# Kernel optimization log

Hardware: AMD Instinct MI355X
Metric: run time of the kernel (lower is better)

Reference implementation:

```python
import jax, jax.numpy as jnp
import numpy as np

DECAY = 0.1
EPS = 1e-5


def setup_inputs() -> dict:
    key = jax.random.key(0)
    k1, k2, k3, k4 = jax.random.split(key, 4)
    N, K, D = 262144, 1024, 64
    x = jax.random.normal(k1, (N, D), dtype=jnp.float32)
    embed = jax.random.normal(k2, (K, D), dtype=jnp.float32) * 0.01
    cluster_size = jax.random.uniform(k3, (K,), dtype=jnp.float32)
    embed_avg = jax.random.normal(k4, (K, D), dtype=jnp.float32) * 0.01
    return {"x": x, "embed": embed, "cluster_size": cluster_size, "embed_avg": embed_avg}


def reference(x, embed, cluster_size, embed_avg):
    # x: [N, D] flattened latents; embed: [K, D] codebook
    N, D = x.shape
    K = embed.shape[0]

    # Squared Euclidean distance (same argmin as torch.cdist p=2).
    x2 = jnp.sum(x * x, axis=-1, keepdims=True)            # [N, 1]
    e2 = jnp.sum(embed * embed, axis=-1)                   # [K]
    dist = x2 - 2.0 * jnp.einsum('nd,kd->nk', x, embed) + e2[None, :]  # [N, K]
    embed_ind = jnp.argmin(dist, axis=-1)                  # [N] int

    # Quantize: gather nearest codes.
    quantize = embed[embed_ind]                            # [N, D]

    # --- EMA codebook update (no-grad in the original) ---
    xs = jax.lax.stop_gradient(x)
    bins = jax.ops.segment_sum(jnp.ones((N,), dtype=x.dtype), embed_ind,
                               num_segments=K)             # [K] bincount
    embed_sum = jax.ops.segment_sum(xs, embed_ind, num_segments=K)  # [K, D] scatter-add

    cluster_size_new = cluster_size * DECAY + bins * (1.0 - DECAY)
    embed_avg_new = embed_avg * DECAY + embed_sum * (1.0 - DECAY)

    # Laplace smoothing then normalize to get the updated codebook.
    n = jnp.sum(cluster_size_new)
    cs_smoothed = (cluster_size_new + EPS) / (n + K * EPS) * n
    embed_normalized = embed_avg_new / cs_smoothed[:, None]  # [K, D]

    return quantize, embed_ind, cluster_size_new, embed_avg_new, embed_normalized
```

## Files before the change

### kernel.cpp

```cpp
#include <hip/hip_runtime.h>
#include <hip/hip_bf16.h>


#define NROWS 262144
#define KCODES 1024
#define DDIM 64
#define CAPL 8

typedef __attribute__((ext_vector_type(8)))  short short8;
typedef __attribute__((ext_vector_type(16))) float f32x16;

__device__ __forceinline__ unsigned short f2bf(float f) {
    unsigned u = __float_as_uint(f);
    unsigned r = u + 0x7fffu + ((u >> 16) & 1u);
    return (unsigned short)(r >> 16);
}

__global__ __launch_bounds__(256) void vq_prep(
    const float* __restrict__ embed, unsigned short* __restrict__ eb,
    float* __restrict__ e2f, float* __restrict__ enmax2)
{
    const int k = blockIdx.x * 256 + threadIdx.x;
    const float* er = embed + (size_t)k * DDIM;
    float s = 0.f;
    #pragma unroll
    for (int d = 0; d < DDIM; ++d) { float v = er[d]; s = fmaf(v, v, s); }
    e2f[k] = s;
    #pragma unroll
    for (int d = 0; d < DDIM; ++d) eb[(size_t)k * DDIM + d] = f2bf(er[d]);
    atomicMax((int*)enmax2, __float_as_int(s));
}

#define STAGE(H)                                                              \
    _Pragma("unroll")                                                         \
    for (int it = 0; it < 8; ++it) {                                          \
        const int f16  = t + it * 512;                                        \
        const int ch   = f16 >> 8;                                            \
        const int r    = f16 & 255;                                           \
        const int code = r >> 3, slot = r & 7;                                \
        const short8 v = *reinterpret_cast<const short8*>(                    \
            eb + (size_t)(H) * 32768 + (size_t)f16 * 8);                      \
        *reinterpret_cast<short8*>((char*)ebs + ch * 4096 + code * 128 +      \
                                   ((slot ^ (code & 7)) << 4)) = v;           \
    }

#define SWEEP1(E2ARR)                                                         \
    _Pragma("unroll")                                                         \
    for (int ch = 0; ch < 16; ++ch) {                                         \
        short8 bfr[4];                                                        \
        _Pragma("unroll")                                                     \
        for (int i = 0; i < 4; ++i) {                                         \
            const int slot = 2 * i + hi;                                      \
            bfr[i] = *reinterpret_cast<const short8*>(                        \
                (char*)ebs + ch * 4096 + lo * 128 + ((slot ^ (lo & 7)) << 4));\
        }                                                                     \
        const float e2l = E2ARR[ch];                                          \
        f32x16 acc;                                                           \
        _Pragma("unroll")                                                     \
        for (int r = 0; r < 16; ++r) acc[r] = 0.f;                            \
        _Pragma("unroll")                                                     \
        for (int i = 0; i < 4; ++i)                                           \
            acc = __builtin_amdgcn_mfma_f32_32x32x16_bf16(af[i], bfr[i], acc, 0, 0, 0); \
        _Pragma("unroll")                                                     \
        for (int r = 0; r < 16; ++r)                                          \
            best[r] = fminf(best[r], fmaf(-2.f, acc[r], e2l));                \
    }

#define SWEEP2(E2ARR, CBASE)                                                  \
    _Pragma("unroll")                                                         \
    for (int ch = 0; ch < 16; ++ch) {                                         \
        short8 bfr[4];                                                        \
        _Pragma("unroll")                                                     \
        for (int i = 0; i < 4; ++i) {                                         \
            const int slot = 2 * i + hi;                                      \
            bfr[i] = *reinterpret_cast<const short8*>(                        \
                (char*)ebs + ch * 4096 + lo * 128 + ((slot ^ (lo & 7)) << 4));\
        }                                                                     \
        const float e2l = E2ARR[ch];                                          \
        f32x16 acc;                                                           \
        _Pragma("unroll")                                                     \
        for (int r = 0; r < 16; ++r) acc[r] = 0.f;                            \
        _Pragma("unroll")                                                     \
        for (int i = 0; i < 4; ++i)                                           \
            acc = __builtin_amdgcn_mfma_f32_32x32x16_bf16(af[i], bfr[i], acc, 0, 0, 0); \
        _Pragma("unroll")                                                     \
        for (int r = 0; r < 16; ++r) {                                        \
            const float d0 = fmaf(-2.f, acc[r], e2l);                         \
            if (d0 <= best[r]) {                                              \
                const int rr = (r & 3) + 8 * (r >> 2) + 4 * hi;               \
                const int rl = wid * 32 + rr;                                 \
                const int idx = atomicAdd(&cntL[rl], 1);                      \
                if (idx < CAPL) candL[rl][idx] = (CBASE) + ch * 32 + lo;      \
            }                                                                 \
        }                                                                     \
    }

__global__ __launch_bounds__(512, 4) void vq_phaseA(
    const float* __restrict__ x, const unsigned short* __restrict__ eb,
    const float* __restrict__ e2f, const float* __restrict__ enmax2,
    float* __restrict__ out_ind, int* __restrict__ candg, int* __restrict__ cntg,
    int* __restrict__ wl, int* __restrict__ gcount,
    int* __restrict__ wl2, int* __restrict__ gcount2, int* __restrict__ bins_i)
{
    __shared__ __align__(16) unsigned short ebs[32768];
    __shared__ float norm2L[256];
    __shared__ int   cntL[256];
    __shared__ int   candL[256][CAPL];
    __shared__ int   mcount, mbase, mcount2, mbase2;

    const int t    = threadIdx.x;
    const int lane = t & 63;
    const int wid  = t >> 6;
    const int lo   = lane & 31;
    const int hi   = lane >> 5;
    const int rowb = blockIdx.x * 256;
    const int myrow = rowb + wid * 32 + lo;

    short8 af[4];
    float xsq = 0.f;
    {
        const float* xr = x + (size_t)myrow * DDIM;
        #pragma unroll
        for (int i = 0; i < 4; ++i) {
            const float4 a = *reinterpret_cast<const float4*>(xr + 16 * i + 8 * hi);
            const float4 b = *reinterpret_cast<const float4*>(xr + 16 * i + 8 * hi + 4);
            short8 f;
            f[0] = (short)f2bf(a.x); f[1] = (short)f2bf(a.y);
            f[2] = (short)f2bf(a.z); f[3] = (short)f2bf(a.w);
            f[4] = (short)f2bf(b.x); f[5] = (short)f2bf(b.y);
            f[6] = (short)f2bf(b.z); f[7] = (short)f2bf(b.w);
            af[i] = f;
            xsq = fmaf(a.x, a.x, xsq); xsq = fmaf(a.y, a.y, xsq);
            xsq = fmaf(a.z, a.z, xsq); xsq = fmaf(a.w, a.w, xsq);
            xsq = fmaf(b.x, b.x, xsq); xsq = fmaf(b.y, b.y, xsq);
            xsq = fmaf(b.z, b.z, xsq); xsq = fmaf(b.w, b.w, xsq);
        }
    }
    const float n2full = xsq + __shfl_xor(xsq, 32);
    if (hi == 0) norm2L[wid * 32 + lo] = n2full;

    float e2h0[16], e2h1[16];
    #pragma unroll
    for (int c = 0; c < 16; ++c) e2h0[c] = e2f[c * 32 + lo];
    #pragma unroll
    for (int c = 0; c < 16; ++c) e2h1[c] = e2f[(16 + c) * 32 + lo];

    if (t < 256) cntL[t] = 0;
    if (t == 0) { mcount = 0; mcount2 = 0; }
    const float en2 = *enmax2;

    f32x16 best;
    #pragma unroll
    for (int r = 0; r < 16; ++r) best[r] = 3.4e38f;

    STAGE(0)
    __syncthreads();
    SWEEP1(e2h0)
    __syncthreads();
    STAGE(1)
    __syncthreads();
    SWEEP1(e2h1)

    #pragma unroll
    for (int r = 0; r < 16; ++r) {
        float v = best[r];
        v = fminf(v, __shfl_xor(v, 1));  v = fminf(v, __shfl_xor(v, 2));
        v = fminf(v, __shfl_xor(v, 4));  v = fminf(v, __shfl_xor(v, 8));
        v = fminf(v, __shfl_xor(v, 16));
        const int rr = (r & 3) + 8 * (r >> 2) + 4 * hi;
        const float nr2 = norm2L[wid * 32 + rr];
        best[r] = v + 0.015625f * sqrtf(nr2 * en2) + 1e-4f;
    }

    SWEEP2(e2h1, 512)
    __syncthreads();
    STAGE(0)
    __syncthreads();
    SWEEP2(e2h0, 0)
    __syncthreads();

    int my = -1, my2 = -1, c = 0;
    if (t < 256) {
        c = cntL[t];
        if (c == 1) {
            const int code = candL[t][0];
            out_ind[rowb + t] = (float)code;
            atomicAdd(bins_i + code, 1);
        }
        else if (c <= CAPL)   my  = atomicAdd(&mcount, 1);
        else                  my2 = atomicAdd(&mcount2, 1);
    }
    __syncthreads();
    if (t == 0) { mbase = atomicAdd(gcount, mcount); mbase2 = atomicAdd(gcount2, mcount2); }
    __syncthreads();
    if (my >= 0) {
        const int row = rowb + t;
        wl[mbase + my] = row;
        cntg[row] = c;
        #pragma unroll
        for (int j = 0; j < CAPL; ++j)
            if (j < c) candg[row * 8 + j] = candL[t][j];
    }
    if (my2 >= 0) wl2[mbase2 + my2] = rowb + t;
}

__global__ __launch_bounds__(256) void vq_rerank1(
    const float* __restrict__ x, const float* __restrict__ embed,
    const float* __restrict__ e2f, const int* __restrict__ wl,
    const int* __restrict__ gcount, const int* __restrict__ cntg,
    const int* __restrict__ candg, float* __restrict__ out_ind,
    int* __restrict__ bins_i)
{
    const int n = *gcount;
    for (int i = blockIdx.x * 256 + threadIdx.x; i < n; i += gridDim.x * 256) {
        const int row = wl[i];
        float xv[DDIM];
        {
            const float4* xp = reinterpret_cast<const float4*>(x + (size_t)row * DDIM);
            float4 xq[16];
            #pragma unroll
            for (int q = 0; q < 16; ++q) xq[q] = xp[q];
            #pragma unroll
            for (int q = 0; q < 16; ++q) {
                xv[q*4+0] = xq[q].x; xv[q*4+1] = xq[q].y;
                xv[q*4+2] = xq[q].z; xv[q*4+3] = xq[q].w;
            }
        }
        float x2 = 0.f;
        #pragma unroll
        for (int d = 0; d < DDIM; ++d) x2 = fmaf(xv[d], xv[d], x2);

        const int c = cntg[row];
        float bv = 3.4e38f; int bk = 0x7fffffff;
        for (int ci = 0; ci < c; ++ci) {
            const int k = candg[row * 8 + ci];
            const float4* ep = reinterpret_cast<const float4*>(embed + (size_t)k * DDIM);
            float dot = 0.f;
            #pragma unroll
            for (int q = 0; q < 16; ++q) {
                const float4 e4 = ep[q];
                dot = fmaf(xv[q*4+0], e4.x, dot);
                dot = fmaf(xv[q*4+1], e4.y, dot);
                dot = fmaf(xv[q*4+2], e4.z, dot);
                dot = fmaf(xv[q*4+3], e4.w, dot);
            }
            const float dist = (x2 - 2.0f * dot) + e2f[k];
            if (dist < bv || (dist == bv && k < bk)) { bv = dist; bk = k; }
        }
        out_ind[row] = (float)bk;
        atomicAdd(bins_i + bk, 1);
    }
}

__global__ __launch_bounds__(256) void vq_rerank2(
    const float* __restrict__ x, const float* __restrict__ embed,
    const float* __restrict__ e2f, const int* __restrict__ wl2,
    const int* __restrict__ gcount2, float* __restrict__ out_ind,
    int* __restrict__ bins_i)
{
    const int t    = threadIdx.x;
    const int lane = t & 63;
    const int gw   = (blockIdx.x * 256 + t) >> 6;
    const int nw   = (gridDim.x * 256) >> 6;
    const int n    = *gcount2;

    for (int e = gw; e < n; e += nw) {
        const int row = wl2[e];
        float xv[DDIM];
        {
            const float4* xp = reinterpret_cast<const float4*>(x + (size_t)row * DDIM);
            #pragma unroll
            for (int q = 0; q < 16; ++q) {
                const float4 v = xp[q];
                xv[q*4+0] = v.x; xv[q*4+1] = v.y; xv[q*4+2] = v.z; xv[q*4+3] = v.w;
            }
        }
        float x2 = 0.f;
        #pragma unroll
        for (int d = 0; d < DDIM; ++d) x2 = fmaf(xv[d], xv[d], x2);

        float bv = 3.4e38f; int bk = 0x7fffffff;
        for (int k = lane; k < KCODES; k += 64) {
            const float* er = embed + (size_t)k * DDIM;
            float dot = 0.f;
            #pragma unroll
            for (int d = 0; d < DDIM; ++d) dot = fmaf(xv[d], er[d], dot);
            const float dist = (x2 - 2.0f * dot) + e2f[k];
            if (dist < bv) { bv = dist; bk = k; }
        }
        #pragma unroll
        for (int s = 1; s < 64; s <<= 1) {
            const float ov = __shfl_xor(bv, s);
            const int   ok = __shfl_xor(bk, s);
            if (ov < bv || (ov == bv && ok < bk)) { bv = ov; bk = ok; }
        }
        if (lane == 0) { out_ind[row] = (float)bk; atomicAdd(bins_i + bk, 1); }
    }
}

__global__ __launch_bounds__(1024) void vq_prefix(
    const int* __restrict__ bins_i, int* __restrict__ offs, int* __restrict__ cursor)
{
    __shared__ int s[KCODES];
    const int t = threadIdx.x;
    const int b = bins_i[t];
    s[t] = b;
    __syncthreads();
    for (int d = 1; d < KCODES; d <<= 1) {
        const int v = (t >= d) ? s[t - d] : 0;
        __syncthreads();
        s[t] += v;
        __syncthreads();
    }
    const int excl = s[t] - b;
    offs[t] = excl;
    cursor[t] = excl;
}

__global__ __launch_bounds__(256) void vq_scatter(
    const float* __restrict__ out_ind, int* __restrict__ cursor, int* __restrict__ sorted)
{
    const int row  = blockIdx.x * 256 + threadIdx.x;
    const int code = (int)out_ind[row];
    const int pos  = atomicAdd(cursor + code, 1);
    sorted[pos] = (code << 20) | row;
}

__global__ __launch_bounds__(256) void vq_reduce(
    const float* __restrict__ x, const int* __restrict__ sorted,
    float* __restrict__ esum)
{
    const int t = threadIdx.x, lane = t & 63, w = t >> 6;
    const int p0 = (blockIdx.x * 4 + w) * 64;

    int cur = sorted[p0] >> 20;
    float acc = 0.f;
    #pragma unroll 4
    for (int i = 0; i < 64; i += 4) {
        const int4 e4 = *reinterpret_cast<const int4*>(sorted + p0 + i);
        const float v0 = x[(size_t)(e4.x & 0xFFFFF) * DDIM + lane];
        const float v1 = x[(size_t)(e4.y & 0xFFFFF) * DDIM + lane];
        const float v2 = x[(size_t)(e4.z & 0xFFFFF) * DDIM + lane];
        const float v3 = x[(size_t)(e4.w & 0xFFFFF) * DDIM + lane];
        const int c0 = e4.x >> 20, c1 = e4.y >> 20, c2 = e4.z >> 20, c3 = e4.w >> 20;
        if (c0 != cur) { unsafeAtomicAdd(esum + cur * DDIM + lane, acc); acc = 0.f; cur = c0; }
        acc += v0;
        if (c1 != cur) { unsafeAtomicAdd(esum + cur * DDIM + lane, acc); acc = 0.f; cur = c1; }
        acc += v1;
        if (c2 != cur) { unsafeAtomicAdd(esum + cur * DDIM + lane, acc); acc = 0.f; cur = c2; }
        acc += v2;
        if (c3 != cur) { unsafeAtomicAdd(esum + cur * DDIM + lane, acc); acc = 0.f; cur = c3; }
        acc += v3;
    }
    unsafeAtomicAdd(esum + cur * DDIM + lane, acc);
}

__global__ __launch_bounds__(1024) void vq_finalize(
    const float* __restrict__ cluster_size, const float* __restrict__ embed_avg,
    const int* __restrict__ bins_i, float* __restrict__ out_cs,
    float* __restrict__ out_eavg, float* __restrict__ out_enorm)
{
    __shared__ float red[KCODES];
    __shared__ float css[KCODES];
    const int t = threadIdx.x;

    const float csn = cluster_size[t] * 0.1f + (float)bins_i[t] * 0.9f;
    red[t] = csn;
    __syncthreads();
    for (int s = 512; s > 0; s >>= 1) {
        if (t < s) red[t] += red[t + s];
        __syncthreads();
    }
    const float n = red[0];
    out_cs[t] = csn;
    css[t] = (csn + 1e-5f) / (n + (float)(KCODES * 1e-5)) * n;
    __syncthreads();

    #pragma unroll
    for (int i = 0; i < 16; ++i) {
        const int f4 = t + i * 1024;
        const int k  = f4 >> 4;
        const float4 ea = reinterpret_cast<const float4*>(embed_avg)[f4];
        const float4 su = reinterpret_cast<const float4*>(out_eavg)[f4];
        const float  cc = css[k];
        float4 ean, en;
        ean.x = ea.x * 0.1f + su.x * 0.9f; en.x = ean.x / cc;
        ean.y = ea.y * 0.1f + su.y * 0.9f; en.y = ean.y / cc;
        ean.z = ea.z * 0.1f + su.z * 0.9f; en.z = ean.z / cc;
        ean.w = ea.w * 0.1f + su.w * 0.9f; en.w = ean.w / cc;
        reinterpret_cast<float4*>(out_eavg)[f4]  = ean;
        reinterpret_cast<float4*>(out_enorm)[f4] = en;
    }
}

__global__ __launch_bounds__(256) void vq_quant(
    const float* __restrict__ out_ind, const float* __restrict__ embed,
    float* __restrict__ out_q)
{
    __shared__ int inds[256];
    const int t = threadIdx.x;
    const int row0 = blockIdx.x * 256;
    inds[t] = (int)out_ind[row0 + t];
    __syncthreads();
    #pragma unroll
    for (int i = 0; i < 16; ++i) {
        const int f = t + i * 256;
        const int r = f >> 4, dq = f & 15;
        const int code = inds[r];
        const float4 ev = *reinterpret_cast<const float4*>(
            embed + (size_t)code * DDIM + dq * 4);
        *reinterpret_cast<float4*>(out_q + (size_t)(row0 + r) * DDIM + dq * 4) = ev;
    }
}

extern "C" void kernel_launch(void* const* d_in, const int* in_sizes, int n_in,
                              void* d_out, int out_size, void* d_ws, size_t ws_size,
                              hipStream_t stream)
{
    const float* x            = (const float*)d_in[0];
    const float* embed        = (const float*)d_in[1];
    const float* cluster_size = (const float*)d_in[2];
    const float* embed_avg    = (const float*)d_in[3];

    float* out      = (float*)d_out;
    float* out_q    = out;
    float* out_ind  = out_q + (size_t)NROWS * DDIM;
    float* out_cs   = out_ind + NROWS;
    float* out_eavg = out_cs + KCODES;
    float* out_en   = out_eavg + (size_t)KCODES * DDIM;

    unsigned short* eb = (unsigned short*)out_en;
    float* e2f = out_en + 32768;

    int* S      = (int*)out_q;
    int* candg  = S;
    int* cntg   = S + 2097152;
    int* wl     = S + 2359296;
    int* wl2    = S + 2621440;
    int* sorted = S + 2883584;
    int* bins_i = S + 3145728;
    int* gcount = bins_i + KCODES;
    int* gcount2= gcount + 1;
    float* enmax2 = (float*)(gcount2 + 1);
    int* offs   = gcount2 + 2;
    int* cursor = offs + KCODES;

    hipMemsetAsync(bins_i, 0, (KCODES + 3) * sizeof(int), stream);
    hipMemsetAsync(out_eavg, 0, (size_t)KCODES * DDIM * sizeof(float), stream);

    vq_prep    <<<KCODES / 256, 256, 0, stream>>>(embed, eb, e2f, enmax2);
    vq_phaseA  <<<NROWS / 256, 512, 0, stream>>>(x, eb, e2f, enmax2, out_ind,
                                                 candg, cntg, wl, gcount,
                                                 wl2, gcount2, bins_i);
    vq_rerank1 <<<512, 256, 0, stream>>>(x, embed, e2f, wl, gcount, cntg, candg,
                                         out_ind, bins_i);
    vq_rerank2 <<<128, 256, 0, stream>>>(x, embed, e2f, wl2, gcount2, out_ind, bins_i);
    vq_prefix  <<<1, 1024, 0, stream>>>(bins_i, offs, cursor);
    vq_scatter <<<NROWS / 256, 256, 0, stream>>>(out_ind, cursor, sorted);
    vq_reduce  <<<NROWS / 256, 256, 0, stream>>>(x, sorted, out_eavg);
    vq_finalize<<<1, 1024, 0, stream>>>(cluster_size, embed_avg, bins_i,
                                        out_cs, out_eavg, out_en);
    vq_quant   <<<NROWS / 256, 256, 0, stream>>>(out_ind, embed, out_q);
}
```

Before: 310.5 us.

## Process two row tiles per wave in VQ phase A to reuse codebook fragments

Each wave now handles 64 rows instead of 32, so every codebook fragment loaded from LDS feeds two MFMA chains. This halves LDS reads per row and halves the number of blocks. The distance is reformulated as a maximum of dot minus half the code norm, with the half norm preloaded into the accumulator, which removes the per-element fma. The candidate margin is halved to match the rescaled quantity and the per-row candidate cap drops from 8 to 4, sending more rows to the slower rerank2 path. Register pressure roughly doubles for the A fragments and best arrays, which may lower occupancy.

```diff
diff --git a/kernel.cpp b/kernel.cpp
--- a/kernel.cpp
+++ b/kernel.cpp
@@ -5,7 +5,7 @@
 #define NROWS 262144
 #define KCODES 1024
 #define DDIM 64
-#define CAPL 8
+#define CAPL 4
 
 typedef __attribute__((ext_vector_type(8)))  short short8;
 typedef __attribute__((ext_vector_type(16))) float f32x16;
@@ -30,70 +30,6 @@
     for (int d = 0; d < DDIM; ++d) eb[(size_t)k * DDIM + d] = f2bf(er[d]);
     atomicMax((int*)enmax2, __float_as_int(s));
 }
-
-#define STAGE(H)                                                              \
-    _Pragma("unroll")                                                         \
-    for (int it = 0; it < 8; ++it) {                                          \
-        const int f16  = t + it * 512;                                        \
-        const int ch   = f16 >> 8;                                            \
-        const int r    = f16 & 255;                                           \
-        const int code = r >> 3, slot = r & 7;                                \
-        const short8 v = *reinterpret_cast<const short8*>(                    \
-            eb + (size_t)(H) * 32768 + (size_t)f16 * 8);                      \
-        *reinterpret_cast<short8*>((char*)ebs + ch * 4096 + code * 128 +      \
-                                   ((slot ^ (code & 7)) << 4)) = v;           \
-    }
-
-#define SWEEP1(E2ARR)                                                         \
-    _Pragma("unroll")                                                         \
-    for (int ch = 0; ch < 16; ++ch) {                                         \
-        short8 bfr[4];                                                        \
-        _Pragma("unroll")                                                     \
-        for (int i = 0; i < 4; ++i) {                                         \
-            const int slot = 2 * i + hi;                                      \
-            bfr[i] = *reinterpret_cast<const short8*>(                        \
-                (char*)ebs + ch * 4096 + lo * 128 + ((slot ^ (lo & 7)) << 4));\
-        }                                                                     \
-        const float e2l = E2ARR[ch];                                          \
-        f32x16 acc;                                                           \
-        _Pragma("unroll")                                                     \
-        for (int r = 0; r < 16; ++r) acc[r] = 0.f;                            \
-        _Pragma("unroll")                                                     \
-        for (int i = 0; i < 4; ++i)                                           \
-            acc = __builtin_amdgcn_mfma_f32_32x32x16_bf16(af[i], bfr[i], acc, 0, 0, 0); \
-        _Pragma("unroll")                                                     \
-        for (int r = 0; r < 16; ++r)                                          \
-            best[r] = fminf(best[r], fmaf(-2.f, acc[r], e2l));                \
-    }
-
-#define SWEEP2(E2ARR, CBASE)                                                  \
-    _Pragma("unroll")                                                         \
-    for (int ch = 0; ch < 16; ++ch) {                                         \
-        short8 bfr[4];                                                        \
-        _Pragma("unroll")                                                     \
-        for (int i = 0; i < 4; ++i) {                                         \
-            const int slot = 2 * i + hi;                                      \
-            bfr[i] = *reinterpret_cast<const short8*>(                        \
-                (char*)ebs + ch * 4096 + lo * 128 + ((slot ^ (lo & 7)) << 4));\
-        }                                                                     \
-        const float e2l = E2ARR[ch];                                          \
-        f32x16 acc;                                                           \
-        _Pragma("unroll")                                                     \
-        for (int r = 0; r < 16; ++r) acc[r] = 0.f;                            \
-        _Pragma("unroll")                                                     \
-        for (int i = 0; i < 4; ++i)                                           \
-            acc = __builtin_amdgcn_mfma_f32_32x32x16_bf16(af[i], bfr[i], acc, 0, 0, 0); \
-        _Pragma("unroll")                                                     \
-        for (int r = 0; r < 16; ++r) {                                        \
-            const float d0 = fmaf(-2.f, acc[r], e2l);                         \
-            if (d0 <= best[r]) {                                              \
-                const int rr = (r & 3) + 8 * (r >> 2) + 4 * hi;               \
-                const int rl = wid * 32 + rr;                                 \
-                const int idx = atomicAdd(&cntL[rl], 1);                      \
-                if (idx < CAPL) candL[rl][idx] = (CBASE) + ch * 32 + lo;      \
-            }                                                                 \
-        }                                                                     \
-    }
 
 __global__ __launch_bounds__(512, 4) void vq_phaseA(
     const float* __restrict__ x, const unsigned short* __restrict__ eb,
@@ -103,9 +39,10 @@
     int* __restrict__ wl2, int* __restrict__ gcount2, int* __restrict__ bins_i)
 {
     __shared__ __align__(16) unsigned short ebs[32768];
-    __shared__ float norm2L[256];
-    __shared__ int   cntL[256];
-    __shared__ int   candL[256][CAPL];
+    __shared__ float e2L[512];
+    __shared__ float norm2L[512];
+    __shared__ int   cntL[512];
+    __shared__ int   candL[512][CAPL];
     __shared__ int   mcount, mbase, mcount2, mbase2;
 
     const int t    = threadIdx.x;
@@ -113,13 +50,12 @@
     const int wid  = t >> 6;
     const int lo   = lane & 31;
     const int hi   = lane >> 5;
-    const int rowb = blockIdx.x * 256;
-    const int myrow = rowb + wid * 32 + lo;
-
-    short8 af[4];
-    float xsq = 0.f;
+    const int rowb = blockIdx.x * 512;
+
+    short8 af0[4], af1[4];
     {
-        const float* xr = x + (size_t)myrow * DDIM;
+        const float* xr = x + (size_t)(rowb + wid * 64 + lo) * DDIM;
+        float xsq = 0.f;
         #pragma unroll
         for (int i = 0; i < 4; ++i) {
             const float4 a = *reinterpret_cast<const float4*>(xr + 16 * i + 8 * hi);
@@ -129,67 +65,145 @@
             f[2] = (short)f2bf(a.z); f[3] = (short)f2bf(a.w);
             f[4] = (short)f2bf(b.x); f[5] = (short)f2bf(b.y);
             f[6] = (short)f2bf(b.z); f[7] = (short)f2bf(b.w);
-            af[i] = f;
+            af0[i] = f;
             xsq = fmaf(a.x, a.x, xsq); xsq = fmaf(a.y, a.y, xsq);
             xsq = fmaf(a.z, a.z, xsq); xsq = fmaf(a.w, a.w, xsq);
             xsq = fmaf(b.x, b.x, xsq); xsq = fmaf(b.y, b.y, xsq);
             xsq = fmaf(b.z, b.z, xsq); xsq = fmaf(b.w, b.w, xsq);
         }
-    }
-    const float n2full = xsq + __shfl_xor(xsq, 32);
-    if (hi == 0) norm2L[wid * 32 + lo] = n2full;
-
-    float e2h0[16], e2h1[16];
-    #pragma unroll
-    for (int c = 0; c < 16; ++c) e2h0[c] = e2f[c * 32 + lo];
-    #pragma unroll
-    for (int c = 0; c < 16; ++c) e2h1[c] = e2f[(16 + c) * 32 + lo];
-
-    if (t < 256) cntL[t] = 0;
+        const float n2 = xsq + __shfl_xor(xsq, 32);
+        if (hi == 0) norm2L[wid * 64 + lo] = n2;
+    }
+    {
+        const float* xr = x + (size_t)(rowb + wid * 64 + 32 + lo) * DDIM;
+        float xsq = 0.f;
+        #pragma unroll
+        for (int i = 0; i < 4; ++i) {
+            const float4 a = *reinterpret_cast<const float4*>(xr + 16 * i + 8 * hi);
+            const float4 b = *reinterpret_cast<const float4*>(xr + 16 * i + 8 * hi + 4);
+            short8 f;
+            f[0] = (short)f2bf(a.x); f[1] = (short)f2bf(a.y);
+            f[2] = (short)f2bf(a.z); f[3] = (short)f2bf(a.w);
+            f[4] = (short)f2bf(b.x); f[5] = (short)f2bf(b.y);
+            f[6] = (short)f2bf(b.z); f[7] = (short)f2bf(b.w);
+            af1[i] = f;
+            xsq = fmaf(a.x, a.x, xsq); xsq = fmaf(a.y, a.y, xsq);
+            xsq = fmaf(a.z, a.z, xsq); xsq = fmaf(a.w, a.w, xsq);
+            xsq = fmaf(b.x, b.x, xsq); xsq = fmaf(b.y, b.y, xsq);
+            xsq = fmaf(b.z, b.z, xsq); xsq = fmaf(b.w, b.w, xsq);
+        }
+        const float n2 = xsq + __shfl_xor(xsq, 32);
+        if (hi == 0) norm2L[wid * 64 + 32 + lo] = n2;
+    }
+
+    cntL[t] = 0;
     if (t == 0) { mcount = 0; mcount2 = 0; }
     const float en2 = *enmax2;
 
-    f32x16 best;
-    #pragma unroll
-    for (int r = 0; r < 16; ++r) best[r] = 3.4e38f;
+    f32x16 best0, best1;
+    #pragma unroll
+    for (int r = 0; r < 16; ++r) { best0[r] = -3.4e38f; best1[r] = -3.4e38f; }
+
+#define STAGE(H)                                                              \
+    _Pragma("unroll")                                                         \
+    for (int it = 0; it < 8; ++it) {                                          \
+        const int f16  = t + it * 512;                                        \
+        const int ch   = f16 >> 8;                                            \
+        const int rr_  = f16 & 255;                                           \
+        const int code = rr_ >> 3, slot = rr_ & 7;                            \
+        const short8 v = *reinterpret_cast<const short8*>(                    \
+            eb + (size_t)(H) * 32768 + (size_t)f16 * 8);                      \
+        *reinterpret_cast<short8*>((char*)ebs + ch * 4096 + code * 128 +      \
+                                   ((slot ^ (code & 7)) << 4)) = v;           \
+    }                                                                         \
+    e2L[t] = -0.5f * e2f[(H) * 512 + t];
+
+#define CHUNK(ch, KIND, CBASE)                                                \
+    {                                                                         \
+        short8 bfr[4];                                                        \
+        _Pragma("unroll")                                                     \
+        for (int i = 0; i < 4; ++i) {                                         \
+            const int slot = 2 * i + hi;                                      \
+            bfr[i] = *reinterpret_cast<const short8*>(                        \
+                (char*)ebs + (ch) * 4096 + lo * 128 + ((slot ^ (lo & 7)) << 4)); \
+        }                                                                     \
+        const float e2n = e2L[(ch) * 32 + lo];                                \
+        f32x16 acc0, acc1;                                                    \
+        _Pragma("unroll")                                                     \
+        for (int r = 0; r < 16; ++r) { acc0[r] = e2n; acc1[r] = e2n; }        \
+        _Pragma("unroll")                                                     \
+        for (int i = 0; i < 4; ++i) {                                         \
+            acc0 = __builtin_amdgcn_mfma_f32_32x32x16_bf16(af0[i], bfr[i], acc0, 0, 0, 0); \
+            acc1 = __builtin_amdgcn_mfma_f32_32x32x16_bf16(af1[i], bfr[i], acc1, 0, 0, 0); \
+        }                                                                     \
+        if (KIND == 0) {                                                      \
+            _Pragma("unroll")                                                 \
+            for (int r = 0; r < 16; ++r) {                                    \
+                best0[r] = fmaxf(best0[r], acc0[r]);                          \
+                best1[r] = fmaxf(best1[r], acc1[r]);                          \
+            }                                                                 \
+        } else {                                                              \
+            _Pragma("unroll")                                                 \
+            for (int r = 0; r < 16; ++r) {                                    \
+                if (acc0[r] >= best0[r]) {                                    \
+                    const int rr = (r & 3) + 8 * (r >> 2) + 4 * hi;           \
+                    const int rl = wid * 64 + rr;                             \
+                    const int idx = atomicAdd(&cntL[rl], 1);                  \
+                    if (idx < CAPL) candL[rl][idx] = (CBASE) + (ch) * 32 + lo;\
+                }                                                             \
+                if (acc1[r] >= best1[r]) {                                    \
+                    const int rr = (r & 3) + 8 * (r >> 2) + 4 * hi;           \
+                    const int rl = wid * 64 + 32 + rr;                        \
+                    const int idx = atomicAdd(&cntL[rl], 1);                  \
+                    if (idx < CAPL) candL[rl][idx] = (CBASE) + (ch) * 32 + lo;\
+                }                                                             \
+            }                                                                 \
+        }                                                                     \
+    }
 
     STAGE(0)
     __syncthreads();
-    SWEEP1(e2h0)
+    #pragma unroll 2
+    for (int ch = 0; ch < 16; ++ch) CHUNK(ch, 0, 0)
     __syncthreads();
     STAGE(1)
     __syncthreads();
-    SWEEP1(e2h1)
+    #pragma unroll 2
+    for (int ch = 0; ch < 16; ++ch) CHUNK(ch, 0, 512)
 
     #pragma unroll
     for (int r = 0; r < 16; ++r) {
-        float v = best[r];
-        v = fminf(v, __shfl_xor(v, 1));  v = fminf(v, __shfl_xor(v, 2));
-        v = fminf(v, __shfl_xor(v, 4));  v = fminf(v, __shfl_xor(v, 8));
-        v = fminf(v, __shfl_xor(v, 16));
+        float v0 = best0[r], v1 = best1[r];
+        v0 = fmaxf(v0, __shfl_xor(v0, 1));  v1 = fmaxf(v1, __shfl_xor(v1, 1));
+        v0 = fmaxf(v0, __shfl_xor(v0, 2));  v1 = fmaxf(v1, __shfl_xor(v1, 2));
+        v0 = fmaxf(v0, __shfl_xor(v0, 4));  v1 = fmaxf(v1, __shfl_xor(v1, 4));
+        v0 = fmaxf(v0, __shfl_xor(v0, 8));  v1 = fmaxf(v1, __shfl_xor(v1, 8));
+        v0 = fmaxf(v0, __shfl_xor(v0, 16)); v1 = fmaxf(v1, __shfl_xor(v1, 16));
         const int rr = (r & 3) + 8 * (r >> 2) + 4 * hi;
-        const float nr2 = norm2L[wid * 32 + rr];
-        best[r] = v + 0.015625f * sqrtf(nr2 * en2) + 1e-4f;
-    }
-
-    SWEEP2(e2h1, 512)
+        const float m0 = 0.0078125f * sqrtf(norm2L[wid * 64 + rr] * en2) + 5e-5f;
+        const float m1 = 0.0078125f * sqrtf(norm2L[wid * 64 + 32 + rr] * en2) + 5e-5f;
+        best0[r] = v0 - m0;
+        best1[r] = v1 - m1;
+    }
+
+    #pragma unroll 2
+    for (int ch = 0; ch < 16; ++ch) CHUNK(ch, 1, 512)
     __syncthreads();
     STAGE(0)
     __syncthreads();
-    SWEEP2(e2h0, 0)
-    __syncthreads();
-
-    int my = -1, my2 = -1, c = 0;
-    if (t < 256) {
-        c = cntL[t];
-        if (c == 1) {
-            const int code = candL[t][0];
-            out_ind[rowb + t] = (float)code;
-            atomicAdd(bins_i + code, 1);
-        }
-        else if (c <= CAPL)   my  = atomicAdd(&mcount, 1);
-        else                  my2 = atomicAdd(&mcount2, 1);
-    }
+    #pragma unroll 2
+    for (int ch = 0; ch < 16; ++ch) CHUNK(ch, 1, 0)
+    __syncthreads();
+
+    int my = -1, my2 = -1;
+    const int c = cntL[t];
+    if (c == 1) {
+        const int code = candL[t][0];
+        out_ind[rowb + t] = (float)code;
+        atomicAdd(bins_i + code, 1);
+    }
+    else if (c <= CAPL)   my  = atomicAdd(&mcount, 1);
+    else                  my2 = atomicAdd(&mcount2, 1);
     __syncthreads();
     if (t == 0) { mbase = atomicAdd(gcount, mcount); mbase2 = atomicAdd(gcount2, mcount2); }
     __syncthreads();
@@ -199,9 +213,11 @@
         cntg[row] = c;
         #pragma unroll
         for (int j = 0; j < CAPL; ++j)
-            if (j < c) candg[row * 8 + j] = candL[t][j];
+            if (j < c) candg[row * CAPL + j] = candL[t][j];
     }
     if (my2 >= 0) wl2[mbase2 + my2] = rowb + t;
+#undef STAGE
+#undef CHUNK
 }
 
 __global__ __launch_bounds__(256) void vq_rerank1(
@@ -233,7 +249,7 @@
         const int c = cntg[row];
         float bv = 3.4e38f; int bk = 0x7fffffff;
         for (int ci = 0; ci < c; ++ci) {
-            const int k = candg[row * 8 + ci];
+            const int k = candg[row * CAPL + ci];
             const float4* ep = reinterpret_cast<const float4*>(embed + (size_t)k * DDIM);
             float dot = 0.f;
             #pragma unroll
@@ -434,11 +450,11 @@
 
     int* S      = (int*)out_q;
     int* candg  = S;
-    int* cntg   = S + 2097152;
-    int* wl     = S + 2359296;
-    int* wl2    = S + 2621440;
-    int* sorted = S + 2883584;
-    int* bins_i = S + 3145728;
+    int* cntg   = S + 1048576;
+    int* wl     = S + 1310720;
+    int* wl2    = S + 1572864;
+    int* sorted = S + 1835008;
+    int* bins_i = S + 2097152;
     int* gcount = bins_i + KCODES;
     int* gcount2= gcount + 1;
     float* enmax2 = (float*)(gcount2 + 1);
@@ -449,7 +465,7 @@
     hipMemsetAsync(out_eavg, 0, (size_t)KCODES * DDIM * sizeof(float), stream);
 
     vq_prep    <<<KCODES / 256, 256, 0, stream>>>(embed, eb, e2f, enmax2);
-    vq_phaseA  <<<NROWS / 256, 512, 0, stream>>>(x, eb, e2f, enmax2, out_ind,
+    vq_phaseA  <<<NROWS / 512, 512, 0, stream>>>(x, eb, e2f, enmax2, out_ind,
                                                  candg, cntg, wl, gcount,
                                                  wl2, gcount2, bins_i);
     vq_rerank1 <<<512, 256, 0, stream>>>(x, embed, e2f, wl, gcount, cntg, candg,
```

Measured after the change: 410.1 us. 1.32x slower.
